# Optimization experiments

Measured on AMD Instinct MI355X. Metric: run time of the kernel, lower is better.

Reference implementation:

```python
import jax, jax.numpy as jnp
import numpy as np
import math

B, S, HID, H = 2, 4096, 512, 8
D_K = HID // H


def setup_inputs() -> dict:
    key = jax.random.key(0)
    ks = jax.random.split(key, 8)
    inp = {
        "query": jax.random.normal(ks[0], (B, S, HID), dtype=jnp.float32),
        "key": jax.random.normal(ks[1], (B, S, HID), dtype=jnp.float32),
        "value": jax.random.normal(ks[2], (B, S, HID), dtype=jnp.float32),
        "mask": jax.random.randint(ks[3], (B, S), 0, 2, dtype=jnp.int32),
        # conv1d kernel_size=1, bias=False -> plain [out,in] weights (xavier-normal-ish)
        "Wq": jax.random.normal(ks[4], (HID, HID), dtype=jnp.float32) * (1.0 / math.sqrt(HID)),
        "Wk": jax.random.normal(ks[5], (HID, HID), dtype=jnp.float32) * (1.0 / math.sqrt(HID)),
        "Wv": jax.random.normal(ks[6], (HID, HID), dtype=jnp.float32) * (1.0 / math.sqrt(HID)),
        "Wo": jax.random.normal(ks[7], (HID, HID), dtype=jnp.float32) * (1.0 / math.sqrt(HID)),
    }
    return inp


def reference(query, key, value, mask, Wq, Wk, Wv, Wo):
    b, s, _ = query.shape
    # conv1d(k=1, bias=False) projection == x @ W.T; split heads -> [b,h,s,d_k]
    def proj(x, W):
        return jnp.einsum('bsd,ed->bse', x, W).reshape(b, s, H, D_K).transpose(0, 2, 1, 3)
    q, k, v = proj(query, Wq), proj(key, Wk), proj(value, Wv)
    # NOTE: original scales by 1/log(d_k), not 1/sqrt(d_k)
    score = jnp.einsum('bhqd,bhkd->bhqk', q, k) / math.log(D_K)
    m = mask.reshape(b, 1, 1, s)  # broadcast over heads and query positions
    score = jnp.where(m == 0, jnp.float32(-1e30), score)
    attn = jax.nn.softmax(score, axis=-1)  # dropout is identity in eval
    x = jnp.einsum('bhqk,bhkd->bhqd', attn, v)
    x = x.transpose(0, 2, 1, 3).reshape(b, s, HID)
    return jnp.einsum('bsd,ed->bse', x, Wo)
```

## Files before the change

### kernel.cpp

```cpp
#include <hip/hip_runtime.h>
#include <hip/hip_bf16.h>
#include <cstdint>
#include <cstddef>


namespace {

constexpr int kB = 2, kS = 4096, kHid = 512, kH = 8, kDk = 64;
constexpr int kBH = kB * kH;
constexpr int kM = kB * kS;

typedef __attribute__((ext_vector_type(8))) short short8;
typedef __attribute__((ext_vector_type(4))) float floatx4;
typedef unsigned short u16;

__device__ __forceinline__ u16 bf16rne(float f) {
    uint32_t u = __float_as_uint(f);
    u += 0x7fffu + ((u >> 16) & 1u);
    return (u16)(u >> 16);
}
__device__ __forceinline__ uint32_t pk2(float lo, float hi) {
#if __has_builtin(__builtin_amdgcn_cvt_pk_bf16_f32)
    typedef __attribute__((ext_vector_type(2))) __bf16 bf2;
    bf2 h = __builtin_amdgcn_cvt_pk_bf16_f32(lo, hi);
    return __builtin_bit_cast(uint32_t, h);
#else
    return ((uint32_t)bf16rne(hi) << 16) | (uint32_t)bf16rne(lo);
#endif
}
__device__ __forceinline__ float fexp2(float x) {
#if __has_builtin(__builtin_amdgcn_exp2f)
    return __builtin_amdgcn_exp2f(x);
#else
    return exp2f(x);
#endif
}

__global__ __launch_bounds__(256) void cvt_qw(const float* __restrict__ q,
    const float* __restrict__ k, const float* __restrict__ v,
    const float* __restrict__ w0, const float* __restrict__ w1,
    const float* __restrict__ w2, const float* __restrict__ w3,
    u16* __restrict__ xall, u16* __restrict__ wall) {
    const int bx = blockIdx.x;
    if (bx < 12288) {
        int z = bx >> 12;
        size_t i = (size_t)(bx & 4095) * 256 + threadIdx.x;
        const float* src = z == 0 ? q : (z == 1 ? k : v);
        float4 f = ((const float4*)src)[i];
        ushort4 o;
        o.x = bf16rne(f.x); o.y = bf16rne(f.y);
        o.z = bf16rne(f.z); o.w = bf16rne(f.w);
        ((ushort4*)(xall + (size_t)z * kM * kHid))[i] = o;
    } else {
        int r = bx - 12288;
        int z = r >> 8;
        size_t i = (size_t)(r & 255) * 256 + threadIdx.x;
        const float* src = z == 0 ? w0 : (z == 1 ? w1 : (z == 2 ? w2 : w3));
        float sc = (z == 0)
            ? (float)(1.4426950408889634 / (6.0 * 0.6931471805599453))
            : 1.0f;
        float4 f = ((const float4*)src)[i];
        ushort4 o;
        o.x = bf16rne(f.x * sc); o.y = bf16rne(f.y * sc);
        o.z = bf16rne(f.z * sc); o.w = bf16rne(f.w * sc);
        ((ushort4*)(wall + (size_t)z * kHid * kHid))[i] = o;
    }
}

__global__ __launch_bounds__(256) void cvt_mask(const int* __restrict__ mask,
    float* __restrict__ fb) {
    int i = blockIdx.x * 256 + threadIdx.x;
    fb[i] = mask[i] ? 0.0f : -1e30f;
}

__global__ __launch_bounds__(256, 3) void proj(const u16* __restrict__ xall,
    const u16* __restrict__ wall, u16* __restrict__ qp, u16* __restrict__ kp,
    u16* __restrict__ vt) {
    __shared__ float smt[4][16][68];
    const int z = blockIdx.z;
    const u16* x = xall + (size_t)z * kM * kHid;
    const u16* w = wall + (size_t)z * kHid * kHid;
    const int wv = threadIdx.x >> 6, lane = threadIdx.x & 63;
    const int quad = lane >> 4, l16 = lane & 15;
    const int mb = blockIdx.y * 128 + (wv >> 1) * 64;
    const int nb = blockIdx.x * 128 + (wv & 1) * 64;
    floatx4 acc[4][4] = {};
    const u16* xr = x + (size_t)(mb + l16) * kHid + quad * 8;
    const u16* wr = w + (size_t)(nb + l16) * kHid + quad * 8;
    for (int k0 = 0; k0 < kHid; k0 += 32) {
        short8 a[4], bt[4];
#pragma unroll
        for (int i = 0; i < 4; i++)
            a[i] = *(const short8*)(xr + (size_t)i * 16 * kHid + k0);
#pragma unroll
        for (int t = 0; t < 4; t++)
            bt[t] = *(const short8*)(wr + (size_t)t * 16 * kHid + k0);
#pragma unroll
        for (int i = 0; i < 4; i++)
#pragma unroll
        for (int t = 0; t < 4; t++)
            acc[i][t] = __builtin_amdgcn_mfma_f32_16x16x32_bf16(a[i], bt[t], acc[i][t], 0, 0, 0);
    }
    if (z < 2) {
        u16* dst = (z == 0) ? qp : kp;
        const int row16 = lane >> 2, cseg = (lane & 3) * 16;
#pragma unroll
        for (int i = 0; i < 4; i++) {
#pragma unroll
            for (int t = 0; t < 4; t++)
#pragma unroll
            for (int r = 0; r < 4; r++)
                smt[wv][quad * 4 + r][t * 16 + l16] = acc[i][t][r];
            __builtin_amdgcn_wave_barrier();
            const float* rp = &smt[wv][row16][cseg];
            float4 f0 = *(const float4*)(rp);
            float4 f1 = *(const float4*)(rp + 4);
            float4 f2 = *(const float4*)(rp + 8);
            float4 f3 = *(const float4*)(rp + 12);
            uint4 o0, o1;
            o0.x = pk2(f0.x, f0.y); o0.y = pk2(f0.z, f0.w);
            o0.z = pk2(f1.x, f1.y); o0.w = pk2(f1.z, f1.w);
            o1.x = pk2(f2.x, f2.y); o1.y = pk2(f2.z, f2.w);
            o1.z = pk2(f3.x, f3.y); o1.w = pk2(f3.z, f3.w);
            u16* dp = dst + (size_t)(mb + i * 16 + row16) * kHid + nb + cseg;
            *(uint4*)dp = o0;
            *(uint4*)(dp + 8) = o1;
            __builtin_amdgcn_wave_barrier();
        }
    } else {
#pragma unroll
        for (int i = 0; i < 4; i++)
#pragma unroll
        for (int t = 0; t < 4; t++) {
            int m0 = mb + i * 16 + quad * 4;
            int n = nb + t * 16 + l16;
            int b = m0 >> 12, s = m0 & (kS - 1);
            int h = n >> 6,   d = n & (kDk - 1);
            ushort4 o;
            o.x = bf16rne(acc[i][t][0]); o.y = bf16rne(acc[i][t][1]);
            o.z = bf16rne(acc[i][t][2]); o.w = bf16rne(acc[i][t][3]);
            *(ushort4*)(vt + ((size_t)(b * kH + h) * kDk + d) * kS + s) = o;
        }
    }
}

__global__ __launch_bounds__(256, 2) void attn(const u16* __restrict__ qp,
    const u16* __restrict__ kp, const u16* __restrict__ vt,
    const float* __restrict__ fbias, u16* __restrict__ xo) {
    union SmT {
        struct { u16 K[2][64][64]; u16 V[2][64][64]; u16 P[4][32][72]; } s;
        float ep[4][32][68];
    };
    __shared__ __align__(16) SmT sm;
    const int tid = threadIdx.x;
    const int wv = tid >> 6, lane = tid & 63;
    const int quad = lane >> 4, l16 = lane & 15;
    const int bh = blockIdx.y, b = bh >> 3, h = bh & 7;
    const int q0 = blockIdx.x * 128 + wv * 32;
    const u16* Qb = qp + (size_t)b * kS * kHid + h * 64;
    const u16* Kb = kp + (size_t)b * kS * kHid + h * 64;
    const u16* Vb = vt + (size_t)bh * kDk * kS;
    const float* fm = fbias + b * kS;

    short8 qf[2][2];
#pragma unroll
    for (int qt = 0; qt < 2; qt++)
#pragma unroll
    for (int hh = 0; hh < 2; hh++)
        qf[qt][hh] = *(const short8*)(Qb + (size_t)(q0 + qt * 16 + l16) * kHid + hh * 32 + quad * 8);

    floatx4 O[2][4] = {};
    float rs[2] = {0.0f, 0.0f};

    const int srow = tid >> 3;
    const int sc   = (tid & 7) * 8;
    const int pc   = ((tid & 7) ^ (srow & 7)) * 8;
    const int cA = (quad ^ (l16 & 7)) * 8;

    short8 rk[2], rv[2];
    rk[0] = *(const short8*)(Kb + (size_t)srow * kHid + sc);
    rk[1] = *(const short8*)(Kb + (size_t)(srow + 32) * kHid + sc);
    rv[0] = *(const short8*)(Vb + (size_t)srow * kS + sc);
    rv[1] = *(const short8*)(Vb + (size_t)(srow + 32) * kS + sc);
    *(short8*)&sm.s.K[0][srow][pc]      = rk[0];
    *(short8*)&sm.s.K[0][srow + 32][pc] = rk[1];
    *(short8*)&sm.s.V[0][srow][pc]      = rv[0];
    *(short8*)&sm.s.V[0][srow + 32][pc] = rv[1];
    rk[0] = *(const short8*)(Kb + (size_t)(64 + srow) * kHid + sc);
    rk[1] = *(const short8*)(Kb + (size_t)(64 + srow + 32) * kHid + sc);
    rv[0] = *(const short8*)(Vb + (size_t)srow * kS + 64 + sc);
    rv[1] = *(const short8*)(Vb + (size_t)(srow + 32) * kS + 64 + sc);
    __syncthreads();

    for (int it = 0; it < 64; ++it) {
        const int p = it & 1;
        const int kt = it * 64;
        *(short8*)&sm.s.K[1 - p][srow][pc]      = rk[0];
        *(short8*)&sm.s.K[1 - p][srow + 32][pc] = rk[1];
        *(short8*)&sm.s.V[1 - p][srow][pc]      = rv[0];
        *(short8*)&sm.s.V[1 - p][srow + 32][pc] = rv[1];
        {
            const int kt2 = ((it + 2) & 63) * 64;
            rk[0] = *(const short8*)(Kb + (size_t)(kt2 + srow) * kHid + sc);
            rk[1] = *(const short8*)(Kb + (size_t)(kt2 + srow + 32) * kHid + sc);
            rv[0] = *(const short8*)(Vb + (size_t)srow * kS + kt2 + sc);
            rv[1] = *(const short8*)(Vb + (size_t)(srow + 32) * kS + kt2 + sc);
        }
        float4 fb[4];
#pragma unroll
        for (int t = 0; t < 4; t++)
            fb[t] = *(const float4*)(fm + kt + t * 16 + quad * 4);
        short8 kf[4][2], vf[4][2];
#pragma unroll
        for (int t = 0; t < 4; t++) {
            kf[t][0] = *(const short8*)&sm.s.K[p][t * 16 + l16][cA];
            kf[t][1] = *(const short8*)&sm.s.K[p][t * 16 + l16][cA ^ 32];
            vf[t][0] = *(const short8*)&sm.s.V[p][t * 16 + l16][cA];
            vf[t][1] = *(const short8*)&sm.s.V[p][t * 16 + l16][cA ^ 32];
        }
#pragma unroll
        for (int qt = 0; qt < 2; qt++) {
            floatx4 st[4];
#pragma unroll
            for (int t = 0; t < 4; t++) {
                floatx4 z = {fb[t].x, fb[t].y, fb[t].z, fb[t].w};
                z = __builtin_amdgcn_mfma_f32_16x16x32_bf16(kf[t][0], qf[qt][0], z, 0, 0, 0);
                st[t] = __builtin_amdgcn_mfma_f32_16x16x32_bf16(kf[t][1], qf[qt][1], z, 0, 0, 0);
            }
            u16* prow = &sm.s.P[wv][qt * 16 + l16][0];
            float sum = 0.0f;
#pragma unroll
            for (int t = 0; t < 4; t++) {
                float p0 = fexp2(st[t][0]);
                float p1 = fexp2(st[t][1]);
                float p2 = fexp2(st[t][2]);
                float p3 = fexp2(st[t][3]);
                sum += (p0 + p1) + (p2 + p3);
                uint2 w2; w2.x = pk2(p0, p1); w2.y = pk2(p2, p3);
                *(uint2*)(prow + t * 16 + quad * 4) = w2;
            }
            rs[qt] += sum;
        }
        __builtin_amdgcn_wave_barrier();
#pragma unroll
        for (int qt = 0; qt < 2; qt++) {
            short8 ap0 = *(const short8*)&sm.s.P[wv][qt * 16 + l16][quad * 8];
            short8 ap1 = *(const short8*)&sm.s.P[wv][qt * 16 + l16][32 + quad * 8];
#pragma unroll
            for (int td = 0; td < 4; td++) {
                O[qt][td] = __builtin_amdgcn_mfma_f32_16x16x32_bf16(vf[td][0], ap0, O[qt][td], 0, 0, 0);
                O[qt][td] = __builtin_amdgcn_mfma_f32_16x16x32_bf16(vf[td][1], ap1, O[qt][td], 0, 0, 0);
            }
        }
        __syncthreads();
    }

    float inv[2];
#pragma unroll
    for (int qt = 0; qt < 2; qt++) {
        float r = rs[qt];
        r += __shfl_xor(r, 16);
        r += __shfl_xor(r, 32);
        inv[qt] = 1.0f / r;
    }
#pragma unroll
    for (int qt = 0; qt < 2; qt++)
#pragma unroll
    for (int td = 0; td < 4; td++) {
        floatx4 o4 = O[qt][td];
        o4[0] *= inv[qt]; o4[1] *= inv[qt]; o4[2] *= inv[qt]; o4[3] *= inv[qt];
        *(floatx4*)&sm.ep[wv][qt * 16 + l16][td * 16 + quad * 4] = o4;
    }
    __builtin_amdgcn_wave_barrier();
    {
        const int qloc = lane >> 1, half = lane & 1;
        const float* row = &sm.ep[wv][qloc][half * 32];
        u16* orow = xo + ((size_t)(b * kS + q0 + qloc)) * kHid + h * 64 + half * 32;
#pragma unroll
        for (int j = 0; j < 4; j++) {
            float4 f0 = *(const float4*)(row + j * 8);
            float4 f1 = *(const float4*)(row + j * 8 + 4);
            uint4 o;
            o.x = pk2(f0.x, f0.y); o.y = pk2(f0.z, f0.w);
            o.z = pk2(f1.x, f1.y); o.w = pk2(f1.z, f1.w);
            *(uint4*)(orow + j * 8) = o;
        }
    }
}

__global__ __launch_bounds__(256, 3) void oproj(const u16* __restrict__ x,
    const u16* __restrict__ w, float* __restrict__ out) {
    const int wv = threadIdx.x >> 6, lane = threadIdx.x & 63;
    const int quad = lane >> 4, l16 = lane & 15;
    const int mb = blockIdx.y * 128 + (wv >> 1) * 64;
    const int nb = blockIdx.x * 128 + (wv & 1) * 64;
    floatx4 acc[4][4] = {};
    const u16* xr = x + (size_t)(mb + l16) * kHid + quad * 8;
    const u16* wr = w + (size_t)(nb + l16) * kHid + quad * 8;
    for (int k0 = 0; k0 < kHid; k0 += 32) {
        short8 a[4], bt[4];
#pragma unroll
        for (int i = 0; i < 4; i++)
            a[i] = *(const short8*)(xr + (size_t)i * 16 * kHid + k0);
#pragma unroll
        for (int t = 0; t < 4; t++)
            bt[t] = *(const short8*)(wr + (size_t)t * 16 * kHid + k0);
#pragma unroll
        for (int i = 0; i < 4; i++)
#pragma unroll
        for (int t = 0; t < 4; t++)
            acc[i][t] = __builtin_amdgcn_mfma_f32_16x16x32_bf16(a[i], bt[t], acc[i][t], 0, 0, 0);
    }
#pragma unroll
    for (int i = 0; i < 4; i++)
#pragma unroll
    for (int t = 0; t < 4; t++)
#pragma unroll
    for (int r = 0; r < 4; r++) {
        int m = mb + i * 16 + quad * 4 + r;
        int n = nb + t * 16 + l16;
        out[(size_t)m * kHid + n] = acc[i][t][r];
    }
}

}

extern "C" void kernel_launch(void* const* d_in, const int* in_sizes, int n_in,
                              void* d_out, int out_size, void* d_ws, size_t ws_size,
                              hipStream_t stream) {
    const float* q  = (const float*)d_in[0];
    const float* k  = (const float*)d_in[1];
    const float* v  = (const float*)d_in[2];
    const int* mask = (const int*)d_in[3];
    const float* w0 = (const float*)d_in[4];
    const float* w1 = (const float*)d_in[5];
    const float* w2 = (const float*)d_in[6];
    const float* w3 = (const float*)d_in[7];
    float* out = (float*)d_out;

    u16* ws   = (u16*)d_ws;
    u16* xall = ws;
    u16* wall = xall + (size_t)3 * kM * kHid;
    u16* qp   = wall + (size_t)4 * kHid * kHid;
    u16* kp   = qp + (size_t)kBH * kS * kDk;
    u16* vt   = kp + (size_t)kBH * kS * kDk;
    u16* xo   = xall;
    float* fbias = (float*)(xall + (size_t)kM * kHid);

    dim3 blk(256);
    cvt_qw <<<dim3(13312), blk, 0, stream>>>(q, k, v, w0, w1, w2, w3, xall, wall);
    proj   <<<dim3(kHid / 128, kM / 128, 3), blk, 0, stream>>>(xall, wall, qp, kp, vt);
    cvt_mask<<<dim3(kB * kS / 256), blk, 0, stream>>>(mask, fbias);
    attn   <<<dim3(kS / 128, kBH), blk, 0, stream>>>(qp, kp, vt, fbias, xo);
    oproj  <<<dim3(kHid / 128, kM / 128), blk, 0, stream>>>(
        xo, wall + (size_t)3 * kHid * kHid, out);
}
```

Measured before the change: 271.1 us.

## Fuse fp32-to-bf16 activation conversion into projections and compute V transposed

Removes the separate pass that converted the query, key and value activations to bf16. The projection kernels now load fp32 directly and pack to bf16 in registers, which removes a full write and re-read of the converted activations. The V projection is split into its own kernel that computes W·Xᵀ, so the transposed V output can be written with coalesced 16-byte stores through shared memory instead of scattered ushort4 stores. In exchange, the projections read twice as many activation bytes (fp32 instead of bf16), and the workspace layout is reorganised.

```diff
diff --git a/kernel.cpp b/kernel.cpp
--- a/kernel.cpp
+++ b/kernel.cpp
@@ -12,6 +12,7 @@
 
 typedef __attribute__((ext_vector_type(8))) short short8;
 typedef __attribute__((ext_vector_type(4))) float floatx4;
+typedef __attribute__((ext_vector_type(4))) unsigned int uint4v;
 typedef unsigned short u16;
 
 __device__ __forceinline__ u16 bf16rne(float f) {
@@ -28,6 +29,12 @@
     return ((uint32_t)bf16rne(hi) << 16) | (uint32_t)bf16rne(lo);
 #endif
 }
+__device__ __forceinline__ short8 pk8(float4 f0, float4 f1) {
+    uint4v u;
+    u[0] = pk2(f0.x, f0.y); u[1] = pk2(f0.z, f0.w);
+    u[2] = pk2(f1.x, f1.y); u[3] = pk2(f1.z, f1.w);
+    return __builtin_bit_cast(short8, u);
+}
 __device__ __forceinline__ float fexp2(float x) {
 #if __has_builtin(__builtin_amdgcn_exp2f)
     return __builtin_amdgcn_exp2f(x);
@@ -36,35 +43,20 @@
 #endif
 }
 
-__global__ __launch_bounds__(256) void cvt_qw(const float* __restrict__ q,
-    const float* __restrict__ k, const float* __restrict__ v,
-    const float* __restrict__ w0, const float* __restrict__ w1,
-    const float* __restrict__ w2, const float* __restrict__ w3,
-    u16* __restrict__ xall, u16* __restrict__ wall) {
-    const int bx = blockIdx.x;
-    if (bx < 12288) {
-        int z = bx >> 12;
-        size_t i = (size_t)(bx & 4095) * 256 + threadIdx.x;
-        const float* src = z == 0 ? q : (z == 1 ? k : v);
-        float4 f = ((const float4*)src)[i];
-        ushort4 o;
-        o.x = bf16rne(f.x); o.y = bf16rne(f.y);
-        o.z = bf16rne(f.z); o.w = bf16rne(f.w);
-        ((ushort4*)(xall + (size_t)z * kM * kHid))[i] = o;
-    } else {
-        int r = bx - 12288;
-        int z = r >> 8;
-        size_t i = (size_t)(r & 255) * 256 + threadIdx.x;
-        const float* src = z == 0 ? w0 : (z == 1 ? w1 : (z == 2 ? w2 : w3));
-        float sc = (z == 0)
-            ? (float)(1.4426950408889634 / (6.0 * 0.6931471805599453))
-            : 1.0f;
-        float4 f = ((const float4*)src)[i];
-        ushort4 o;
-        o.x = bf16rne(f.x * sc); o.y = bf16rne(f.y * sc);
-        o.z = bf16rne(f.z * sc); o.w = bf16rne(f.w * sc);
-        ((ushort4*)(wall + (size_t)z * kHid * kHid))[i] = o;
-    }
+__global__ __launch_bounds__(256) void cvt_w(const float* __restrict__ w0,
+    const float* __restrict__ w1, const float* __restrict__ w2,
+    const float* __restrict__ w3, u16* __restrict__ wall) {
+    int z = blockIdx.x >> 8;
+    size_t i = (size_t)(blockIdx.x & 255) * 256 + threadIdx.x;
+    const float* src = z == 0 ? w0 : (z == 1 ? w1 : (z == 2 ? w2 : w3));
+    float sc = (z == 0)
+        ? (float)(1.4426950408889634 / (6.0 * 0.6931471805599453))
+        : 1.0f;
+    float4 f = ((const float4*)src)[i];
+    ushort4 o;
+    o.x = bf16rne(f.x * sc); o.y = bf16rne(f.y * sc);
+    o.z = bf16rne(f.z * sc); o.w = bf16rne(f.w * sc);
+    ((ushort4*)(wall + (size_t)z * kHid * kHid))[i] = o;
 }
 
 __global__ __launch_bounds__(256) void cvt_mask(const int* __restrict__ mask,
@@ -73,25 +65,28 @@
     fb[i] = mask[i] ? 0.0f : -1e30f;
 }
 
-__global__ __launch_bounds__(256, 3) void proj(const u16* __restrict__ xall,
-    const u16* __restrict__ wall, u16* __restrict__ qp, u16* __restrict__ kp,
-    u16* __restrict__ vt) {
+__global__ __launch_bounds__(256, 3) void proj_qk(const float* __restrict__ xq,
+    const float* __restrict__ xk, const u16* __restrict__ wall,
+    u16* __restrict__ qp, u16* __restrict__ kp) {
     __shared__ float smt[4][16][68];
     const int z = blockIdx.z;
-    const u16* x = xall + (size_t)z * kM * kHid;
+    const float* x = z ? xk : xq;
     const u16* w = wall + (size_t)z * kHid * kHid;
+    u16* dst = z ? kp : qp;
     const int wv = threadIdx.x >> 6, lane = threadIdx.x & 63;
     const int quad = lane >> 4, l16 = lane & 15;
     const int mb = blockIdx.y * 128 + (wv >> 1) * 64;
     const int nb = blockIdx.x * 128 + (wv & 1) * 64;
     floatx4 acc[4][4] = {};
-    const u16* xr = x + (size_t)(mb + l16) * kHid + quad * 8;
+    const float* xr = x + (size_t)(mb + l16) * kHid + quad * 8;
     const u16* wr = w + (size_t)(nb + l16) * kHid + quad * 8;
     for (int k0 = 0; k0 < kHid; k0 += 32) {
         short8 a[4], bt[4];
 #pragma unroll
-        for (int i = 0; i < 4; i++)
-            a[i] = *(const short8*)(xr + (size_t)i * 16 * kHid + k0);
+        for (int i = 0; i < 4; i++) {
+            const float* p = xr + (size_t)i * 16 * kHid + k0;
+            a[i] = pk8(*(const float4*)p, *(const float4*)(p + 4));
+        }
 #pragma unroll
         for (int t = 0; t < 4; t++)
             bt[t] = *(const short8*)(wr + (size_t)t * 16 * kHid + k0);
@@ -101,46 +96,84 @@
         for (int t = 0; t < 4; t++)
             acc[i][t] = __builtin_amdgcn_mfma_f32_16x16x32_bf16(a[i], bt[t], acc[i][t], 0, 0, 0);
     }
-    if (z < 2) {
-        u16* dst = (z == 0) ? qp : kp;
-        const int row16 = lane >> 2, cseg = (lane & 3) * 16;
-#pragma unroll
-        for (int i = 0; i < 4; i++) {
-#pragma unroll
-            for (int t = 0; t < 4; t++)
-#pragma unroll
-            for (int r = 0; r < 4; r++)
-                smt[wv][quad * 4 + r][t * 16 + l16] = acc[i][t][r];
-            __builtin_amdgcn_wave_barrier();
-            const float* rp = &smt[wv][row16][cseg];
-            float4 f0 = *(const float4*)(rp);
-            float4 f1 = *(const float4*)(rp + 4);
-            float4 f2 = *(const float4*)(rp + 8);
-            float4 f3 = *(const float4*)(rp + 12);
-            uint4 o0, o1;
-            o0.x = pk2(f0.x, f0.y); o0.y = pk2(f0.z, f0.w);
-            o0.z = pk2(f1.x, f1.y); o0.w = pk2(f1.z, f1.w);
-            o1.x = pk2(f2.x, f2.y); o1.y = pk2(f2.z, f2.w);
-            o1.z = pk2(f3.x, f3.y); o1.w = pk2(f3.z, f3.w);
-            u16* dp = dst + (size_t)(mb + i * 16 + row16) * kHid + nb + cseg;
-            *(uint4*)dp = o0;
-            *(uint4*)(dp + 8) = o1;
-            __builtin_amdgcn_wave_barrier();
-        }
-    } else {
-#pragma unroll
-        for (int i = 0; i < 4; i++)
+    const int row16 = lane >> 2, cseg = (lane & 3) * 16;
+#pragma unroll
+    for (int i = 0; i < 4; i++) {
+#pragma unroll
+        for (int t = 0; t < 4; t++)
+#pragma unroll
+        for (int r = 0; r < 4; r++)
+            smt[wv][quad * 4 + r][t * 16 + l16] = acc[i][t][r];
+        __builtin_amdgcn_wave_barrier();
+        const float* rp = &smt[wv][row16][cseg];
+        float4 f0 = *(const float4*)(rp);
+        float4 f1 = *(const float4*)(rp + 4);
+        float4 f2 = *(const float4*)(rp + 8);
+        float4 f3 = *(const float4*)(rp + 12);
+        uint4 o0, o1;
+        o0.x = pk2(f0.x, f0.y); o0.y = pk2(f0.z, f0.w);
+        o0.z = pk2(f1.x, f1.y); o0.w = pk2(f1.z, f1.w);
+        o1.x = pk2(f2.x, f2.y); o1.y = pk2(f2.z, f2.w);
+        o1.z = pk2(f3.x, f3.y); o1.w = pk2(f3.z, f3.w);
+        u16* dp = dst + (size_t)(mb + i * 16 + row16) * kHid + nb + cseg;
+        *(uint4*)dp = o0;
+        *(uint4*)(dp + 8) = o1;
+        __builtin_amdgcn_wave_barrier();
+    }
+}
+
+__global__ __launch_bounds__(256, 3) void proj_v(const float* __restrict__ xv,
+    const u16* __restrict__ wall, u16* __restrict__ vt) {
+    __shared__ float smt[4][16][68];
+    const u16* w = wall + (size_t)2 * kHid * kHid;
+    const int wv = threadIdx.x >> 6, lane = threadIdx.x & 63;
+    const int quad = lane >> 4, l16 = lane & 15;
+    const int mb = blockIdx.y * 128 + (wv >> 1) * 64;
+    const int nbg = blockIdx.x * 128 + (wv & 1) * 64;
+    const int b = nbg >> 12, s0 = nbg & (kS - 1);
+    floatx4 acc[4][4] = {};
+    const u16* ar = w + (size_t)(mb + l16) * kHid + quad * 8;
+    const float* br = xv + (size_t)(nbg + l16) * kHid + quad * 8;
+    for (int k0 = 0; k0 < kHid; k0 += 32) {
+        short8 a[4], bt[4];
+#pragma unroll
+        for (int i = 0; i < 4; i++)
+            a[i] = *(const short8*)(ar + (size_t)i * 16 * kHid + k0);
 #pragma unroll
         for (int t = 0; t < 4; t++) {
-            int m0 = mb + i * 16 + quad * 4;
-            int n = nb + t * 16 + l16;
-            int b = m0 >> 12, s = m0 & (kS - 1);
-            int h = n >> 6,   d = n & (kDk - 1);
-            ushort4 o;
-            o.x = bf16rne(acc[i][t][0]); o.y = bf16rne(acc[i][t][1]);
-            o.z = bf16rne(acc[i][t][2]); o.w = bf16rne(acc[i][t][3]);
-            *(ushort4*)(vt + ((size_t)(b * kH + h) * kDk + d) * kS + s) = o;
-        }
+            const float* p = br + (size_t)t * 16 * kHid + k0;
+            bt[t] = pk8(*(const float4*)p, *(const float4*)(p + 4));
+        }
+#pragma unroll
+        for (int i = 0; i < 4; i++)
+#pragma unroll
+        for (int t = 0; t < 4; t++)
+            acc[i][t] = __builtin_amdgcn_mfma_f32_16x16x32_bf16(a[i], bt[t], acc[i][t], 0, 0, 0);
+    }
+    const int row16 = lane >> 2, cseg = (lane & 3) * 16;
+    u16* dstb = vt + (size_t)b * kHid * kS;
+#pragma unroll
+    for (int i = 0; i < 4; i++) {
+#pragma unroll
+        for (int t = 0; t < 4; t++)
+#pragma unroll
+        for (int r = 0; r < 4; r++)
+            smt[wv][quad * 4 + r][t * 16 + l16] = acc[i][t][r];
+        __builtin_amdgcn_wave_barrier();
+        const float* rp = &smt[wv][row16][cseg];
+        float4 f0 = *(const float4*)(rp);
+        float4 f1 = *(const float4*)(rp + 4);
+        float4 f2 = *(const float4*)(rp + 8);
+        float4 f3 = *(const float4*)(rp + 12);
+        uint4 o0, o1;
+        o0.x = pk2(f0.x, f0.y); o0.y = pk2(f0.z, f0.w);
+        o0.z = pk2(f1.x, f1.y); o0.w = pk2(f1.z, f1.w);
+        o1.x = pk2(f2.x, f2.y); o1.y = pk2(f2.z, f2.w);
+        o1.z = pk2(f3.x, f3.y); o1.w = pk2(f3.z, f3.w);
+        u16* dp = dstb + (size_t)(mb + i * 16 + row16) * kS + s0 + cseg;
+        *(uint4*)dp = o0;
+        *(uint4*)(dp + 8) = o1;
+        __builtin_amdgcn_wave_barrier();
     }
 }
 
@@ -339,18 +372,18 @@
     float* out = (float*)d_out;
 
     u16* ws   = (u16*)d_ws;
-    u16* xall = ws;
-    u16* wall = xall + (size_t)3 * kM * kHid;
+    u16* xo   = ws;
+    u16* wall = xo + (size_t)kM * kHid;
     u16* qp   = wall + (size_t)4 * kHid * kHid;
-    u16* kp   = qp + (size_t)kBH * kS * kDk;
-    u16* vt   = kp + (size_t)kBH * kS * kDk;
-    u16* xo   = xall;
-    float* fbias = (float*)(xall + (size_t)kM * kHid);
+    u16* kp   = qp + (size_t)kM * kHid;
+    u16* vt   = kp + (size_t)kM * kHid;
+    float* fbias = (float*)(vt + (size_t)kM * kHid);
 
     dim3 blk(256);
-    cvt_qw <<<dim3(13312), blk, 0, stream>>>(q, k, v, w0, w1, w2, w3, xall, wall);
-    proj   <<<dim3(kHid / 128, kM / 128, 3), blk, 0, stream>>>(xall, wall, qp, kp, vt);
+    cvt_w  <<<dim3(1024), blk, 0, stream>>>(w0, w1, w2, w3, wall);
     cvt_mask<<<dim3(kB * kS / 256), blk, 0, stream>>>(mask, fbias);
+    proj_qk<<<dim3(kHid / 128, kM / 128, 2), blk, 0, stream>>>(q, k, wall, qp, kp);
+    proj_v <<<dim3(kM / 128, kHid / 128), blk, 0, stream>>>(v, wall, vt);
     attn   <<<dim3(kS / 128, kBH), blk, 0, stream>>>(qp, kp, vt, fbias, xo);
     oproj  <<<dim3(kHid / 128, kM / 128), blk, 0, stream>>>(
         xo, wall + (size_t)3 * kHid * kHid, out);
```

New measurement: 313.7 us. 1.16x slower.
